# Kernel tuning notes

Hardware: AMD Instinct MI355X
Metric: run time of the kernel (lower is better)

The kernel has to match this reference:

```python
import jax, jax.numpy as jnp
import numpy as np

E = 16          # embed_dim
EPS = 1e-5      # BatchNorm eps


def _lin(x, w, b):
    # torch nn.Linear: y = x @ W^T + b
    return x @ w.T + b


def _mha_len1(v, in_w, in_b, out_w, out_b):
    # nn.MultiheadAttention with query/key/value of seq_len 1:
    # softmax over a single key is identically 1, so the output is
    # out_proj(v_proj(value)) and is independent of query/key.
    wv, bv = in_w[2 * E:3 * E], in_b[2 * E:3 * E]
    return _lin(_lin(v, wv, bv), out_w, out_b)


def _forward(x, ehr_w, ehr_b, img_w, img_b, bio_w, bio_b,
             bio_qkv_w, bio_qkv_b, ehr_qkv_w, ehr_qkv_b, img_qkv_w, img_qkv_b,
             attn_in_w, attn_in_b, attn_out_w, attn_out_b,
             ab_proj_w, ab_proj_b, f1_w, f1_b, bn_g, bn_b, f2_w, f2_b):
    # per-modality scalar -> embed_dim encoders (seq_len-1, so work in [B,E])
    ehr_feat = jax.nn.relu(_lin(x[:, 0:1], ehr_w, ehr_b))  # [B,E]
    img_feat = jax.nn.relu(_lin(x[:, 1:2], img_w, img_b))
    bio_feat = jax.nn.relu(_lin(x[:, 2:3], bio_w, bio_b))

    # stacked q/k/v projections per modality; only V slices affect the output
    bio_qkv = _lin(bio_feat, bio_qkv_w, bio_qkv_b)  # [B,3E]
    ehr_qkv = _lin(ehr_feat, ehr_qkv_w, ehr_qkv_b)
    img_qkv = _lin(img_feat, img_qkv_w, img_qkv_b)
    Va = bio_qkv[:, 2 * E:3 * E]
    Vb = ehr_qkv[:, 2 * E:3 * E]

    bio_ehr = _mha_len1(Vb, attn_in_w, attn_in_b, attn_out_w, attn_out_b)
    ehr_bio = _mha_len1(Va, attn_in_w, attn_in_b, attn_out_w, attn_out_b)

    ab = _lin(jnp.concatenate([bio_ehr, ehr_bio], axis=-1), ab_proj_w, ab_proj_b)  # [B,E]
    img_ab = _mha_len1(ab, attn_in_w, attn_in_b, attn_out_w, attn_out_b)

    final = jnp.concatenate([ab, img_ab], axis=-1)  # [B,2E]
    h = _lin(final, f1_w, f1_b)                      # [B,64]
    # BatchNorm1d, training-mode batch statistics (biased variance); dropout off
    mu = jnp.mean(h, axis=0)
    var = jnp.mean(jnp.square(h - mu), axis=0)
    h = (h - mu) * jax.lax.rsqrt(var + EPS) * bn_g + bn_b
    h = jax.nn.relu(h)
    return _lin(h, f2_w, f2_b)  # [B,3]


def setup_inputs() -> dict:
    key = jax.random.key(0)
    ks = iter(jax.random.split(key, 40))
    w = lambda *shape: jax.random.normal(next(ks), shape, jnp.float32) * 0.1
    B = 1048576
    return {
        "x": jax.random.normal(next(ks), (B, 3), jnp.float32),
        "ehr_w": w(E, 1), "ehr_b": w(E),
        "img_w": w(E, 1), "img_b": w(E),
        "bio_w": w(E, 1), "bio_b": w(E),
        "bio_qkv_w": w(3 * E, E), "bio_qkv_b": w(3 * E),
        "ehr_qkv_w": w(3 * E, E), "ehr_qkv_b": w(3 * E),
        "img_qkv_w": w(3 * E, E), "img_qkv_b": w(3 * E),
        "attn_in_w": w(3 * E, E), "attn_in_b": w(3 * E),
        "attn_out_w": w(E, E), "attn_out_b": w(E),
        "ab_proj_w": w(E, 2 * E), "ab_proj_b": w(E),
        "f1_w": w(64, 2 * E), "f1_b": w(64),
        "bn_g": jnp.ones((64,), jnp.float32), "bn_b": jnp.zeros((64,), jnp.float32),
        "f2_w": w(3, 64), "f2_b": w(3),
    }


def reference(x, ehr_w, ehr_b, img_w, img_b, bio_w, bio_b,
              bio_qkv_w, bio_qkv_b, ehr_qkv_w, ehr_qkv_b, img_qkv_w, img_qkv_b,
              attn_in_w, attn_in_b, attn_out_w, attn_out_b,
              ab_proj_w, ab_proj_b, f1_w, f1_b, bn_g, bn_b, f2_w, f2_b):
    return _forward(x, ehr_w, ehr_b, img_w, img_b, bio_w, bio_b,
                    bio_qkv_w, bio_qkv_b, ehr_qkv_w, ehr_qkv_b, img_qkv_w, img_qkv_b,
                    attn_in_w, attn_in_b, attn_out_w, attn_out_b,
                    ab_proj_w, ab_proj_b, f1_w, f1_b, bn_g, bn_b, f2_w, f2_b)
```

## Files before the change

kernel.cpp:

```cpp
#include <hip/hip_runtime.h>
#include <math.h>

#define NITV 17
#define NCELL (NITV*NITV)
#define NREP 4
#define QS   4096.0f
#define QINV (1.0/4096.0)
#define CELLF 6
#define AGG_N (NCELL*CELLF)
#define PSTRIDE 1760
#define NG 16

#define RAW_OFF   0
#define THR_OFF   4352
#define F2PK_OFF  4384
#define EVT_OFF   4480
#define BVT_OFF   5568
#define ST2_OFF   6656
#define PART_OFF  62976

typedef _Float16 h2 __attribute__((ext_vector_type(2)));

#if __has_builtin(__builtin_amdgcn_fdot2)
__device__ __forceinline__ float fdot2f(h2 a, h2 b, float c) {
  return __builtin_amdgcn_fdot2(a, b, c, false);
}
#else
__device__ __forceinline__ float fdot2f(h2 a, h2 b, float c) {
  return fmaf((float)a.x, (float)b.x, fmaf((float)a.y, (float)b.y, c));
}
#endif

__device__ __forceinline__ int bsearch17(const float* t, float x) {
  bool c8 = t[7] < x;
  float s2 = c8 ? t[11] : t[3];
  bool c4 = s2 < x;
  float sa = c8 ? t[13] : t[5];
  float sb = c8 ? t[9]  : t[1];
  float s3 = c4 ? sa : sb;
  bool c2 = s3 < x;
  float v00 = c2 ? t[2]  : t[0];
  float v01 = c2 ? t[6]  : t[4];
  float v10 = c2 ? t[10] : t[8];
  float v11 = c2 ? t[14] : t[12];
  float w0 = c4 ? v01 : v00;
  float w1 = c4 ? v11 : v10;
  float s4 = c8 ? w1 : w0;
  bool c1 = s4 < x;
  int c = (c8?8:0) + (c4?4:0) + (c2?2:0) + (c1?1:0);
  c += (t[15] < x) ? 1 : 0;
  return c;
}

__global__ void __launch_bounds__(256) hist_kernel(
    const float* __restrict__ x,
    const float* __restrict__ ehr_w, const float* __restrict__ ehr_b,
    const float* __restrict__ bio_w, const float* __restrict__ bio_b,
    const float* __restrict__ bio_qkv_w, const float* __restrict__ bio_qkv_b,
    const float* __restrict__ ehr_qkv_w, const float* __restrict__ ehr_qkv_b,
    const float* __restrict__ attn_in_w, const float* __restrict__ attn_in_b,
    const float* __restrict__ attn_out_w, const float* __restrict__ attn_out_b,
    const float* __restrict__ ab_proj_w, const float* __restrict__ ab_proj_b,
    const float* __restrict__ f1_w, const float* __restrict__ f1_b,
    float* __restrict__ ws, int* __restrict__ partials,
    int B, int nbh)
{
  __shared__ int accS[NREP*AGG_N];
  __shared__ float thrS[32];
  __shared__ float mvec[16], uvec[16], vvec[16], cab[16], h0p[64];
  __shared__ float wEx[16], bEx[16], cEx[16], tEx[16];
  __shared__ float wBx[16], bBx[16], cBx[16], tBx[16];
  __shared__ int   rkE[16], rkB[16];
  const int tid = threadIdx.x;

  if ((int)blockIdx.x == nbh) {
    float* S  = (float*)accS;
    float* M  = S;
    float* P1 = S + 256;
    float* P2 = S + 512;
    float* Ae = S + 768;
    float* Ab = S + 1024;
    float* G  = S + 1280;
    float* Ge = S + 2304;
    float* Gb = S + 3328;

    {
      int o = tid >> 4, k = tid & 15;
      float s = 0.f;
      for (int j = 0; j < 16; ++j)
        s = fmaf(attn_out_w[o*16+j], attn_in_w[(32+j)*16+k], s);
      M[tid] = s;
    }
    if (tid < 16) {
      float s = attn_out_b[tid];
      for (int j = 0; j < 16; ++j)
        s = fmaf(attn_out_w[tid*16+j], attn_in_b[32+j], s);
      mvec[tid] = s;
    }
    __syncthreads();

    {
      int o = tid >> 4, i = tid & 15;
      float s1 = 0.f, s2 = 0.f;
      for (int t = 0; t < 16; ++t) {
        float mt = M[t*16+i];
        s1 = fmaf(ab_proj_w[o*32+t],    mt, s1);
        s2 = fmaf(ab_proj_w[o*32+16+t], mt, s2);
      }
      P1[tid] = s1; P2[tid] = s2;
    }
    if (tid < 16) {
      float su = mvec[tid], sv = mvec[tid];
      for (int i = 0; i < 16; ++i) {
        float mt = M[tid*16+i];
        su = fmaf(mt, ehr_qkv_b[32+i], su);
        sv = fmaf(mt, bio_qkv_b[32+i], sv);
      }
      uvec[tid] = su; vvec[tid] = sv;
    }
    for (int idx = tid; idx < 1024; idx += 256) {
      int j = idx >> 4, k = idx & 15;
      float s = f1_w[j*32+k];
      for (int i = 0; i < 16; ++i)
        s = fmaf(f1_w[j*32+16+i], M[i*16+k], s);
      G[idx] = s;
    }
    __syncthreads();

    {
      int o = tid >> 4, k = tid & 15;
      float s1 = 0.f, s2 = 0.f;
      for (int i = 0; i < 16; ++i) {
        s1 = fmaf(P1[o*16+i], ehr_qkv_w[(32+i)*16+k], s1);
        s2 = fmaf(P2[o*16+i], bio_qkv_w[(32+i)*16+k], s2);
      }
      Ae[tid] = s1; Ab[tid] = s2;
    }
    if (tid < 16) {
      float s = ab_proj_b[tid];
      for (int t = 0; t < 16; ++t) {
        s = fmaf(ab_proj_w[tid*32+t],    uvec[t], s);
        s = fmaf(ab_proj_w[tid*32+16+t], vvec[t], s);
      }
      cab[tid] = s;
    }
    if (tid < 16) {
      float w = ehr_w[tid], b = ehr_b[tid];
      bool z = (w == 0.0f);
      wEx[tid] = z ? 0.f : w;
      bEx[tid] = z ? 0.f : b;
      cEx[tid] = z ? fmaxf(b, 0.f) : 0.f;
      tEx[tid] = z ? __builtin_inff() : (-b / w);
    } else if (tid < 32) {
      int k = tid - 16;
      float w = bio_w[k], b = bio_b[k];
      bool z = (w == 0.0f);
      wBx[k] = z ? 0.f : w;
      bBx[k] = z ? 0.f : b;
      cBx[k] = z ? fmaxf(b, 0.f) : 0.f;
      tBx[k] = z ? __builtin_inff() : (-b / w);
    }
    __syncthreads();

    for (int idx = tid; idx < 1024; idx += 256) {
      int j = idx >> 4, k = idx & 15;
      float s1 = 0.f, s2 = 0.f;
      for (int i = 0; i < 16; ++i) {
        float g = G[j*16+i];
        s1 = fmaf(g, Ae[i*16+k], s1);
        s2 = fmaf(g, Ab[i*16+k], s2);
      }
      Ge[idx] = s1; Gb[idx] = s2;
    }
    if (tid < 64) {
      float s = f1_b[tid];
      for (int i = 0; i < 16; ++i) {
        s = fmaf(G[tid*16+i], cab[i], s);
        s = fmaf(f1_w[tid*32+16+i], mvec[i], s);
      }
      h0p[tid] = s;
    }
    if (tid < 16) {
      int r = 0;
      for (int j = 0; j < 16; ++j)
        r += (tEx[j] < tEx[tid]) || (tEx[j] == tEx[tid] && j < tid);
      rkE[tid] = r;
    } else if (tid < 32) {
      int k = tid - 16, r = 0;
      for (int j = 0; j < 16; ++j)
        r += (tBx[j] < tBx[k]) || (tBx[j] == tBx[k] && j < k);
      rkB[k] = r;
    }
    __syncthreads();

    if (tid < 64) {
      float s = h0p[tid];
      for (int k = 0; k < 16; ++k)
        s += Ge[tid*16+k]*cEx[k] + Gb[tid*16+k]*cBx[k];
      h0p[tid] = s;
    }
    __syncthreads();

    for (int idx = tid; idx < NITV*64; idx += 256) {
      int i = idx >> 6, j = idx & 63;
      float ue = 0.f, ve = 0.f, ub = 0.f, vb = 0.f;
      for (int k = 0; k < 16; ++k) {
        bool actE = (wEx[k] > 0.f) ? (rkE[k] < i) : (rkE[k] >= i);
        bool actB = (wBx[k] > 0.f) ? (rkB[k] < i) : (rkB[k] >= i);
        if (actE) { ue = fmaf(Ge[j*16+k], wEx[k], ue); ve = fmaf(Ge[j*16+k], bEx[k], ve); }
        if (actB) { ub = fmaf(Gb[j*16+k], wBx[k], ub); vb = fmaf(Gb[j*16+k], bBx[k], vb); }
      }
      ws[RAW_OFF + idx]        = ue;
      ws[RAW_OFF + 1088 + idx] = ve + h0p[j];
      ws[RAW_OFF + 2176 + idx] = ub;
      ws[RAW_OFF + 3264 + idx] = vb;
    }
    if (tid < 16) {
      ws[THR_OFF + rkE[tid]]      = tEx[tid];
      ws[THR_OFF + 16 + rkB[tid]] = tBx[tid];
    }
    return;
  }

  if (tid < 16) {
    float tloc[16];
    #pragma unroll
    for (int j = 0; j < 16; ++j) {
      float w = ehr_w[j], b = ehr_b[j];
      tloc[j] = (w == 0.0f) ? __builtin_inff() : (-b / w);
    }
    float mine = tloc[tid];
    int r = 0;
    #pragma unroll
    for (int j = 0; j < 16; ++j)
      r += (tloc[j] < mine) || (tloc[j] == mine && j < tid);
    thrS[r] = mine;
  } else if (tid < 32) {
    int k = tid - 16;
    float tloc[16];
    #pragma unroll
    for (int j = 0; j < 16; ++j) {
      float w = bio_w[j], b = bio_b[j];
      tloc[j] = (w == 0.0f) ? __builtin_inff() : (-b / w);
    }
    float mine = tloc[k];
    int r = 0;
    #pragma unroll
    for (int j = 0; j < 16; ++j)
      r += (tloc[j] < mine) || (tloc[j] == mine && j < k);
    thrS[16 + r] = mine;
  }
  for (int i = tid; i < NREP*AGG_N; i += 256) accS[i] = 0;
  __syncthreads();

  float te[16], tb[16];
  #pragma unroll
  for (int k = 0; k < 16; ++k) { te[k] = thrS[k]; tb[k] = thrS[16+k]; }
  const int rep = tid & (NREP-1);
  const int i4max = (B + 3) >> 2;

  for (int i4 = blockIdx.x*256 + tid; i4 < i4max; i4 += nbh*256) {
    const int s0 = i4*4;
    float xs0[4], xs2[4];
    int nv = 0;
    if (s0 + 4 <= B) {
      const float4* xp = (const float4*)(x + (size_t)s0*3);
      float4 a = xp[0], b = xp[1], c = xp[2];
      xs0[0]=a.x; xs2[0]=a.z;  xs0[1]=a.w; xs2[1]=b.y;
      xs0[2]=b.z; xs2[2]=c.x;  xs0[3]=c.y; xs2[3]=c.w;
      nv = 4;
    } else {
      for (int u = 0; u < 4; ++u) {
        int i = s0 + u;
        if (i < B) { xs0[nv] = x[3*(size_t)i]; xs2[nv] = x[3*(size_t)i+2]; ++nv; }
      }
    }
    for (int u = 0; u < nv; ++u) {
      float x0 = xs0[u], x2 = xs2[u];
      int iv0 = bsearch17(te, x0);
      int iv2 = bsearch17(tb, x2);
      int* c = &accS[rep*AGG_N + (iv0*NITV + iv2)*CELLF];
      atomicAdd(c+0, 1);
      atomicAdd(c+1, __float2int_rn(x0*QS));
      atomicAdd(c+2, __float2int_rn(x2*QS));
      atomicAdd(c+3, __float2int_rn(x0*x0*QS));
      atomicAdd(c+4, __float2int_rn(x2*x2*QS));
      atomicAdd(c+5, __float2int_rn(x0*x2*QS));
    }
  }
  __syncthreads();
  int* out = partials + (size_t)blockIdx.x*PSTRIDE;
  for (int i = tid; i < AGG_N; i += 256)
    out[i] = (accS[i] + accS[AGG_N+i]) + (accS[2*AGG_N+i] + accS[3*AGG_N+i]);
}

__global__ void __launch_bounds__(256) reduce_kernel(
    const int* __restrict__ partials, long long* __restrict__ stage2, int nbh)
{
  const int c = blockIdx.x % 7, g = blockIdx.x / 7;
  const int f = c*256 + threadIdx.x;
  if (f >= AGG_N) { if (f < PSTRIDE) stage2[(size_t)g*PSTRIDE + f] = 0; return; }
  long long s = 0;
  for (int b = g; b < nbh; b += NG)
    s += (long long)partials[(size_t)b*PSTRIDE + f];
  stage2[(size_t)g*PSTRIDE + f] = s;
}

__global__ void __launch_bounds__(256) mid_kernel(
    const long long* __restrict__ stage2,
    float* ws, unsigned int* wsu,
    const float* __restrict__ bn_g, const float* __restrict__ bn_b,
    const float* __restrict__ f2_w, int B)
{
  __shared__ double aggd[AGG_N];
  __shared__ float  Rl[4352];
  __shared__ double sh2p[256];
  __shared__ double margnE[NITV], margxE[NITV], margnB[NITV], margxB[NITV];
  __shared__ float  sArr[64], aE[64], aB[64];
  const int tid = threadIdx.x;

  for (int i = tid; i < 1088; i += 256)
    ((uint4*)Rl)[i] = ((const uint4*)(ws + RAW_OFF))[i];
  for (int i = tid; i < AGG_N; i += 256) {
    long long v = 0;
    #pragma unroll
    for (int g = 0; g < NG; ++g) v += stage2[(size_t)g*PSTRIDE + i];
    aggd[i] = (i % CELLF == 0) ? (double)v : (double)v * QINV;
  }
  __syncthreads();

  if (tid < NITV) {
    double n = 0, sx = 0;
    for (int q = 0; q < NITV; ++q) {
      n  += aggd[(tid*NITV+q)*CELLF];
      sx += aggd[(tid*NITV+q)*CELLF + 1];
    }
    margnE[tid] = n; margxE[tid] = sx;
  } else if (tid >= 32 && tid < 32+NITV) {
    int q = tid - 32;
    double n = 0, sx = 0;
    for (int p = 0; p < NITV; ++p) {
      n  += aggd[(p*NITV+q)*CELLF];
      sx += aggd[(p*NITV+q)*CELLF + 2];
    }
    margnB[q] = n; margxB[q] = sx;
  }

  {
    const int j = tid & 63, pg = tid >> 6;
    double sh2 = 0;
    for (int p = pg; p < NITV; p += 4) {
      const double Ue = (double)Rl[p*64+j];
      const double Ve = (double)Rl[1088 + p*64+j];
      for (int q = 0; q < NITV; ++q) {
        const double* c = &aggd[(p*NITV+q)*CELLF];
        double n = c[0], sx0 = c[1], sx2 = c[2], s00 = c[3], s22 = c[4], s02 = c[5];
        double Ub = (double)Rl[2176 + q*64+j];
        double Vb = (double)Rl[3264 + q*64+j];
        sh2 += s00*Ue*Ue + 2.0*sx0*Ue*Ve + n*Ve*Ve
             + s22*Ub*Ub + 2.0*sx2*Ub*Vb + n*Vb*Vb
             + 2.0*(s02*Ue*Ub + sx0*Ue*Vb + sx2*Ve*Ub + n*Ve*Vb);
      }
    }
    sh2p[tid] = sh2;
  }
  __syncthreads();

  if (tid < 64) {
    const int j = tid;
    double sh2 = (sh2p[j] + sh2p[64+j]) + (sh2p[128+j] + sh2p[192+j]);
    const double invB = 1.0 / (double)B;
    double mua = 0, mub = 0;
    for (int p = 0; p < NITV; ++p) {
      mua += margxE[p]*(double)Rl[p*64+j]      + margnE[p]*(double)Rl[1088+p*64+j];
      mub += margxB[p]*(double)Rl[2176+p*64+j] + margnB[p]*(double)Rl[3264+p*64+j];
    }
    mua *= invB; mub *= invB;
    double mu  = mua + mub;
    double var = sh2*invB - mu*mu;
    double s   = (double)bn_g[j] / sqrt(var + 1e-5);
    sArr[j] = (float)s;
    aE[j] = (float)(0.5*(double)bn_b[j] - s*mua);
    aB[j] = (float)(0.5*(double)bn_b[j] - s*mub);
  }
  __syncthreads();

  for (int idx = tid; idx < NITV*32; idx += 256) {
    int itv = idx >> 5, p = idx & 31;
    int j0 = 2*p, j1 = 2*p + 1;
    float sc0 = sArr[j0], sc1 = sArr[j1];
    h2 U, V;
    U.x = (_Float16)(sc0 * Rl[itv*64+j0]);
    U.y = (_Float16)(sc1 * Rl[itv*64+j1]);
    V.x = (_Float16)(fmaf(sc0, Rl[1088+itv*64+j0], aE[j0]));
    V.y = (_Float16)(fmaf(sc1, Rl[1088+itv*64+j1], aE[j1]));
    wsu[EVT_OFF + p*34 + 2*itv]     = __builtin_bit_cast(unsigned int, U);
    wsu[EVT_OFF + p*34 + 2*itv + 1] = __builtin_bit_cast(unsigned int, V);
    U.x = (_Float16)(sc0 * Rl[2176+itv*64+j0]);
    U.y = (_Float16)(sc1 * Rl[2176+itv*64+j1]);
    V.x = (_Float16)(fmaf(sc0, Rl[3264+itv*64+j0], aB[j0]));
    V.y = (_Float16)(fmaf(sc1, Rl[3264+itv*64+j1], aB[j1]));
    wsu[BVT_OFF + p*34 + 2*itv]     = __builtin_bit_cast(unsigned int, U);
    wsu[BVT_OFF + p*34 + 2*itv + 1] = __builtin_bit_cast(unsigned int, V);
  }
  if (tid < 96) {
    int c = tid >> 5, p = tid & 31;
    h2 F;
    F.x = (_Float16)f2_w[c*64 + 2*p];
    F.y = (_Float16)f2_w[c*64 + 2*p + 1];
    wsu[F2PK_OFF + tid] = __builtin_bit_cast(unsigned int, F);
  }
}

__global__ void __launch_bounds__(256) apply_kernel(
    const float* __restrict__ x, const float* __restrict__ ws,
    const unsigned int* __restrict__ wsu,
    const float* __restrict__ f2_b,
    float* __restrict__ out, int B)
{
  __shared__ __align__(16) unsigned int tabs[2176];
  const int tid = threadIdx.x;

  const int s0 = (blockIdx.x*256 + tid)*4;
  float xs0[4], xs2[4];
  int nv = 0;
  if (s0 + 4 <= B) {
    const float4* xp = (const float4*)(x + (size_t)s0*3);
    float4 a = xp[0], b = xp[1], c = xp[2];
    xs0[0]=a.x; xs2[0]=a.z;  xs0[1]=a.w; xs2[1]=b.y;
    xs0[2]=b.z; xs2[2]=c.x;  xs0[3]=c.y; xs2[3]=c.w;
    nv = 4;
  } else {
    for (int u = 0; u < 4; ++u) {
      int i = s0 + u;
      if (i < B) { xs0[nv] = x[3*(size_t)i]; xs2[nv] = x[3*(size_t)i+2]; ++nv; }
    }
  }

  for (int i = tid; i < 544; i += 256)
    ((uint4*)tabs)[i] = ((const uint4*)(wsu + EVT_OFF))[i];

  float te[16], tb[16];
  #pragma unroll
  for (int k = 0; k < 16; ++k) { te[k] = ws[THR_OFF+k]; tb[k] = ws[THR_OFF+16+k]; }
  const h2* f2h = (const h2*)(wsu + F2PK_OFF);
  const float b0 = f2_b[0], b1 = f2_b[1], b2 = f2_b[2];
  __syncthreads();

  h2 hz; hz.x = (_Float16)0.f; hz.y = (_Float16)0.f;
  float res[12];
  #pragma unroll
  for (int u = 0; u < 4; ++u) {
    if (u >= nv) break;
    float x0 = xs0[u], x2 = xs2[u];
    int iv0 = bsearch17(te, x0);
    int iv2 = bsearch17(tb, x2);
    const uint2* ev = ((const uint2*)tabs) + iv0;
    const uint2* bv = ((const uint2*)(tabs + 1088)) + iv2;
    h2 x0h; x0h.x = (_Float16)x0; x0h.y = (_Float16)x0;
    h2 x2h; x2h.x = (_Float16)x2; x2h.y = (_Float16)x2;
    float a0 = b0, a1 = b1, a2 = b2;
    #pragma unroll
    for (int p = 0; p < 32; ++p) {
      uint2 e = ev[p*NITV];
      uint2 v = bv[p*NITV];
      h2 hA = __builtin_elementwise_fma(x0h, __builtin_bit_cast(h2, e.x),
                                              __builtin_bit_cast(h2, e.y));
      h2 hB = __builtin_elementwise_fma(x2h, __builtin_bit_cast(h2, v.x),
                                              __builtin_bit_cast(h2, v.y));
      h2 hh = hA + hB;
      h2 r  = __builtin_elementwise_max(hh, hz);
      a0 = fdot2f(r, f2h[p],      a0);
      a1 = fdot2f(r, f2h[32 + p], a1);
      a2 = fdot2f(r, f2h[64 + p], a2);
    }
    res[u*3+0] = a0; res[u*3+1] = a1; res[u*3+2] = a2;
  }
  if (nv == 4) {
    float4* op = (float4*)(out + (size_t)s0*3);
    op[0] = make_float4(res[0], res[1], res[2],  res[3]);
    op[1] = make_float4(res[4], res[5], res[6],  res[7]);
    op[2] = make_float4(res[8], res[9], res[10], res[11]);
  } else {
    for (int u = 0; u < nv; ++u) {
      size_t i = (size_t)(s0 + u);
      out[3*i+0] = res[u*3+0]; out[3*i+1] = res[u*3+1]; out[3*i+2] = res[u*3+2];
    }
  }
}

extern "C" void kernel_launch(void* const* d_in, const int* in_sizes, int n_in,
                              void* d_out, int out_size, void* d_ws, size_t ws_size,
                              hipStream_t stream) {
  const float* x          = (const float*)d_in[0];
  const float* ehr_w      = (const float*)d_in[1];
  const float* ehr_b      = (const float*)d_in[2];
  const float* bio_w      = (const float*)d_in[5];
  const float* bio_b      = (const float*)d_in[6];
  const float* bio_qkv_w  = (const float*)d_in[7];
  const float* bio_qkv_b  = (const float*)d_in[8];
  const float* ehr_qkv_w  = (const float*)d_in[9];
  const float* ehr_qkv_b  = (const float*)d_in[10];
  const float* attn_in_w  = (const float*)d_in[13];
  const float* attn_in_b  = (const float*)d_in[14];
  const float* attn_out_w = (const float*)d_in[15];
  const float* attn_out_b = (const float*)d_in[16];
  const float* ab_proj_w  = (const float*)d_in[17];
  const float* ab_proj_b  = (const float*)d_in[18];
  const float* f1_w       = (const float*)d_in[19];
  const float* f1_b       = (const float*)d_in[20];
  const float* bn_g       = (const float*)d_in[21];
  const float* bn_b       = (const float*)d_in[22];
  const float* f2_w       = (const float*)d_in[23];
  const float* f2_b       = (const float*)d_in[24];
  float* out = (float*)d_out;
  float* ws  = (float*)d_ws;
  unsigned int* wsu = (unsigned int*)d_ws;
  int* partials = (int*)d_ws + PART_OFF;
  long long* stage2 = (long long*)((int*)d_ws + ST2_OFF);
  const int B = in_sizes[0] / 3;

  long long avail = (long long)(ws_size / 4) - PART_OFF;
  int nbh = (int)(avail / PSTRIDE);
  if (nbh > 1024) nbh = 1024;
  if (nbh < 128)  nbh = 128;

  hist_kernel<<<nbh+1, 256, 0, stream>>>(x, ehr_w, ehr_b, bio_w, bio_b,
      bio_qkv_w, bio_qkv_b, ehr_qkv_w, ehr_qkv_b,
      attn_in_w, attn_in_b, attn_out_w, attn_out_b,
      ab_proj_w, ab_proj_b, f1_w, f1_b, ws, partials, B, nbh);
  reduce_kernel<<<7*NG, 256, 0, stream>>>(partials, stage2, nbh);
  mid_kernel<<<1, 256, 0, stream>>>(stage2, ws, wsu, bn_g, bn_b, f2_w, B);
  apply_kernel<<<(B + 1023)/1024, 256, 0, stream>>>(x, ws, wsu, f2_b, out, B);
}
```

Before: 76.76 us.

## Fuse four-kernel pipeline into one cooperative persistent kernel with grid syncs

```diff
diff --git a/kernel.cpp b/kernel.cpp
--- a/kernel.cpp
+++ b/kernel.cpp
@@ -1,5 +1,8 @@
 #include <hip/hip_runtime.h>
+#include <hip/hip_cooperative_groups.h>
 #include <math.h>
+
+namespace cg = cooperative_groups;
 
 #define NITV 17
 #define NCELL (NITV*NITV)
@@ -52,176 +55,178 @@
   return c;
 }
 
-__global__ void __launch_bounds__(256) hist_kernel(
-    const float* __restrict__ x,
-    const float* __restrict__ ehr_w, const float* __restrict__ ehr_b,
-    const float* __restrict__ bio_w, const float* __restrict__ bio_b,
-    const float* __restrict__ bio_qkv_w, const float* __restrict__ bio_qkv_b,
-    const float* __restrict__ ehr_qkv_w, const float* __restrict__ ehr_qkv_b,
-    const float* __restrict__ attn_in_w, const float* __restrict__ attn_in_b,
-    const float* __restrict__ attn_out_w, const float* __restrict__ attn_out_b,
-    const float* __restrict__ ab_proj_w, const float* __restrict__ ab_proj_b,
-    const float* __restrict__ f1_w, const float* __restrict__ f1_b,
-    float* __restrict__ ws, int* __restrict__ partials,
-    int B, int nbh)
-{
-  __shared__ int accS[NREP*AGG_N];
-  __shared__ float thrS[32];
-  __shared__ float mvec[16], uvec[16], vvec[16], cab[16], h0p[64];
-  __shared__ float wEx[16], bEx[16], cEx[16], tEx[16];
-  __shared__ float wBx[16], bBx[16], cBx[16], tBx[16];
-  __shared__ int   rkE[16], rkB[16];
-  const int tid = threadIdx.x;
-
-  if ((int)blockIdx.x == nbh) {
-    float* S  = (float*)accS;
-    float* M  = S;
-    float* P1 = S + 256;
-    float* P2 = S + 512;
-    float* Ae = S + 768;
-    float* Ab = S + 1024;
-    float* G  = S + 1280;
-    float* Ge = S + 2304;
-    float* Gb = S + 3328;
-
-    {
-      int o = tid >> 4, k = tid & 15;
-      float s = 0.f;
-      for (int j = 0; j < 16; ++j)
-        s = fmaf(attn_out_w[o*16+j], attn_in_w[(32+j)*16+k], s);
-      M[tid] = s;
-    }
-    if (tid < 16) {
-      float s = attn_out_b[tid];
-      for (int j = 0; j < 16; ++j)
-        s = fmaf(attn_out_w[tid*16+j], attn_in_b[32+j], s);
-      mvec[tid] = s;
-    }
-    __syncthreads();
-
-    {
-      int o = tid >> 4, i = tid & 15;
-      float s1 = 0.f, s2 = 0.f;
-      for (int t = 0; t < 16; ++t) {
-        float mt = M[t*16+i];
-        s1 = fmaf(ab_proj_w[o*32+t],    mt, s1);
-        s2 = fmaf(ab_proj_w[o*32+16+t], mt, s2);
-      }
-      P1[tid] = s1; P2[tid] = s2;
-    }
-    if (tid < 16) {
-      float su = mvec[tid], sv = mvec[tid];
-      for (int i = 0; i < 16; ++i) {
-        float mt = M[tid*16+i];
-        su = fmaf(mt, ehr_qkv_b[32+i], su);
-        sv = fmaf(mt, bio_qkv_b[32+i], sv);
-      }
-      uvec[tid] = su; vvec[tid] = sv;
-    }
-    for (int idx = tid; idx < 1024; idx += 256) {
-      int j = idx >> 4, k = idx & 15;
-      float s = f1_w[j*32+k];
-      for (int i = 0; i < 16; ++i)
-        s = fmaf(f1_w[j*32+16+i], M[i*16+k], s);
-      G[idx] = s;
-    }
-    __syncthreads();
-
-    {
-      int o = tid >> 4, k = tid & 15;
-      float s1 = 0.f, s2 = 0.f;
-      for (int i = 0; i < 16; ++i) {
-        s1 = fmaf(P1[o*16+i], ehr_qkv_w[(32+i)*16+k], s1);
-        s2 = fmaf(P2[o*16+i], bio_qkv_w[(32+i)*16+k], s2);
-      }
-      Ae[tid] = s1; Ab[tid] = s2;
-    }
-    if (tid < 16) {
-      float s = ab_proj_b[tid];
-      for (int t = 0; t < 16; ++t) {
-        s = fmaf(ab_proj_w[tid*32+t],    uvec[t], s);
-        s = fmaf(ab_proj_w[tid*32+16+t], vvec[t], s);
-      }
-      cab[tid] = s;
-    }
-    if (tid < 16) {
-      float w = ehr_w[tid], b = ehr_b[tid];
-      bool z = (w == 0.0f);
-      wEx[tid] = z ? 0.f : w;
-      bEx[tid] = z ? 0.f : b;
-      cEx[tid] = z ? fmaxf(b, 0.f) : 0.f;
-      tEx[tid] = z ? __builtin_inff() : (-b / w);
-    } else if (tid < 32) {
-      int k = tid - 16;
-      float w = bio_w[k], b = bio_b[k];
-      bool z = (w == 0.0f);
-      wBx[k] = z ? 0.f : w;
-      bBx[k] = z ? 0.f : b;
-      cBx[k] = z ? fmaxf(b, 0.f) : 0.f;
-      tBx[k] = z ? __builtin_inff() : (-b / w);
-    }
-    __syncthreads();
-
-    for (int idx = tid; idx < 1024; idx += 256) {
-      int j = idx >> 4, k = idx & 15;
-      float s1 = 0.f, s2 = 0.f;
-      for (int i = 0; i < 16; ++i) {
-        float g = G[j*16+i];
-        s1 = fmaf(g, Ae[i*16+k], s1);
-        s2 = fmaf(g, Ab[i*16+k], s2);
-      }
-      Ge[idx] = s1; Gb[idx] = s2;
-    }
-    if (tid < 64) {
-      float s = f1_b[tid];
-      for (int i = 0; i < 16; ++i) {
-        s = fmaf(G[tid*16+i], cab[i], s);
-        s = fmaf(f1_w[tid*32+16+i], mvec[i], s);
-      }
-      h0p[tid] = s;
-    }
-    if (tid < 16) {
-      int r = 0;
-      for (int j = 0; j < 16; ++j)
-        r += (tEx[j] < tEx[tid]) || (tEx[j] == tEx[tid] && j < tid);
-      rkE[tid] = r;
-    } else if (tid < 32) {
-      int k = tid - 16, r = 0;
-      for (int j = 0; j < 16; ++j)
-        r += (tBx[j] < tBx[k]) || (tBx[j] == tBx[k] && j < k);
-      rkB[k] = r;
-    }
-    __syncthreads();
-
-    if (tid < 64) {
-      float s = h0p[tid];
-      for (int k = 0; k < 16; ++k)
-        s += Ge[tid*16+k]*cEx[k] + Gb[tid*16+k]*cBx[k];
-      h0p[tid] = s;
-    }
-    __syncthreads();
-
-    for (int idx = tid; idx < NITV*64; idx += 256) {
-      int i = idx >> 6, j = idx & 63;
-      float ue = 0.f, ve = 0.f, ub = 0.f, vb = 0.f;
-      for (int k = 0; k < 16; ++k) {
-        bool actE = (wEx[k] > 0.f) ? (rkE[k] < i) : (rkE[k] >= i);
-        bool actB = (wBx[k] > 0.f) ? (rkB[k] < i) : (rkB[k] >= i);
-        if (actE) { ue = fmaf(Ge[j*16+k], wEx[k], ue); ve = fmaf(Ge[j*16+k], bEx[k], ve); }
-        if (actB) { ub = fmaf(Gb[j*16+k], wBx[k], ub); vb = fmaf(Gb[j*16+k], bBx[k], vb); }
-      }
-      ws[RAW_OFF + idx]        = ue;
-      ws[RAW_OFF + 1088 + idx] = ve + h0p[j];
-      ws[RAW_OFF + 2176 + idx] = ub;
-      ws[RAW_OFF + 3264 + idx] = vb;
-    }
-    if (tid < 16) {
-      ws[THR_OFF + rkE[tid]]      = tEx[tid];
-      ws[THR_OFF + 16 + rkB[tid]] = tBx[tid];
-    }
-    return;
-  }
-
+
+__device__ void do_setup(unsigned char* smem, int tid,
+    const float* ehr_w, const float* ehr_b, const float* bio_w, const float* bio_b,
+    const float* bio_qkv_w, const float* bio_qkv_b,
+    const float* ehr_qkv_w, const float* ehr_qkv_b,
+    const float* attn_in_w, const float* attn_in_b,
+    const float* attn_out_w, const float* attn_out_b,
+    const float* ab_proj_w, const float* ab_proj_b,
+    const float* f1_w, const float* f1_b, float* ws)
+{
+  float* S  = (float*)smem;
+  float* M  = S;
+  float* P1 = S + 256;
+  float* P2 = S + 512;
+  float* Ae = S + 768;
+  float* Ab = S + 1024;
+  float* G  = S + 1280;
+  float* Ge = S + 2304;
+  float* Gb = S + 3328;
+  float* aux  = (float*)(smem + 17408);
+  float* mvec = aux;        float* uvec = aux + 16;  float* vvec = aux + 32;
+  float* cab  = aux + 48;   float* h0p  = aux + 64;
+  float* wEx  = aux + 128;  float* bEx  = aux + 144; float* cEx = aux + 160;
+  float* tEx  = aux + 176;  float* wBx  = aux + 192; float* bBx = aux + 208;
+  float* cBx  = aux + 224;  float* tBx  = aux + 240;
+  int*   rkE  = (int*)(aux + 256);
+  int*   rkB  = (int*)(aux + 272);
+
+  {
+    int o = tid >> 4, k = tid & 15;
+    float s = 0.f;
+    for (int j = 0; j < 16; ++j)
+      s = fmaf(attn_out_w[o*16+j], attn_in_w[(32+j)*16+k], s);
+    M[tid] = s;
+  }
+  if (tid < 16) {
+    float s = attn_out_b[tid];
+    for (int j = 0; j < 16; ++j)
+      s = fmaf(attn_out_w[tid*16+j], attn_in_b[32+j], s);
+    mvec[tid] = s;
+  }
+  __syncthreads();
+
+  {
+    int o = tid >> 4, i = tid & 15;
+    float s1 = 0.f, s2 = 0.f;
+    for (int t = 0; t < 16; ++t) {
+      float mt = M[t*16+i];
+      s1 = fmaf(ab_proj_w[o*32+t],    mt, s1);
+      s2 = fmaf(ab_proj_w[o*32+16+t], mt, s2);
+    }
+    P1[tid] = s1; P2[tid] = s2;
+  }
+  if (tid < 16) {
+    float su = mvec[tid], sv = mvec[tid];
+    for (int i = 0; i < 16; ++i) {
+      float mt = M[tid*16+i];
+      su = fmaf(mt, ehr_qkv_b[32+i], su);
+      sv = fmaf(mt, bio_qkv_b[32+i], sv);
+    }
+    uvec[tid] = su; vvec[tid] = sv;
+  }
+  for (int idx = tid; idx < 1024; idx += 256) {
+    int j = idx >> 4, k = idx & 15;
+    float s = f1_w[j*32+k];
+    for (int i = 0; i < 16; ++i)
+      s = fmaf(f1_w[j*32+16+i], M[i*16+k], s);
+    G[idx] = s;
+  }
+  __syncthreads();
+
+  {
+    int o = tid >> 4, k = tid & 15;
+    float s1 = 0.f, s2 = 0.f;
+    for (int i = 0; i < 16; ++i) {
+      s1 = fmaf(P1[o*16+i], ehr_qkv_w[(32+i)*16+k], s1);
+      s2 = fmaf(P2[o*16+i], bio_qkv_w[(32+i)*16+k], s2);
+    }
+    Ae[tid] = s1; Ab[tid] = s2;
+  }
+  if (tid < 16) {
+    float s = ab_proj_b[tid];
+    for (int t = 0; t < 16; ++t) {
+      s = fmaf(ab_proj_w[tid*32+t],    uvec[t], s);
+      s = fmaf(ab_proj_w[tid*32+16+t], vvec[t], s);
+    }
+    cab[tid] = s;
+  }
+  if (tid < 16) {
+    float w = ehr_w[tid], b = ehr_b[tid];
+    bool z = (w == 0.0f);
+    wEx[tid] = z ? 0.f : w;
+    bEx[tid] = z ? 0.f : b;
+    cEx[tid] = z ? fmaxf(b, 0.f) : 0.f;
+    tEx[tid] = z ? __builtin_inff() : (-b / w);
+  } else if (tid < 32) {
+    int k = tid - 16;
+    float w = bio_w[k], b = bio_b[k];
+    bool z = (w == 0.0f);
+    wBx[k] = z ? 0.f : w;
+    bBx[k] = z ? 0.f : b;
+    cBx[k] = z ? fmaxf(b, 0.f) : 0.f;
+    tBx[k] = z ? __builtin_inff() : (-b / w);
+  }
+  __syncthreads();
+
+  for (int idx = tid; idx < 1024; idx += 256) {
+    int j = idx >> 4, k = idx & 15;
+    float s1 = 0.f, s2 = 0.f;
+    for (int i = 0; i < 16; ++i) {
+      float g = G[j*16+i];
+      s1 = fmaf(g, Ae[i*16+k], s1);
+      s2 = fmaf(g, Ab[i*16+k], s2);
+    }
+    Ge[idx] = s1; Gb[idx] = s2;
+  }
+  if (tid < 64) {
+    float s = f1_b[tid];
+    for (int i = 0; i < 16; ++i) {
+      s = fmaf(G[tid*16+i], cab[i], s);
+      s = fmaf(f1_w[tid*32+16+i], mvec[i], s);
+    }
+    h0p[tid] = s;
+  }
+  if (tid < 16) {
+    int r = 0;
+    for (int j = 0; j < 16; ++j)
+      r += (tEx[j] < tEx[tid]) || (tEx[j] == tEx[tid] && j < tid);
+    rkE[tid] = r;
+  } else if (tid < 32) {
+    int k = tid - 16, r = 0;
+    for (int j = 0; j < 16; ++j)
+      r += (tBx[j] < tBx[k]) || (tBx[j] == tBx[k] && j < k);
+    rkB[k] = r;
+  }
+  __syncthreads();
+
+  if (tid < 64) {
+    float s = h0p[tid];
+    for (int k = 0; k < 16; ++k)
+      s += Ge[tid*16+k]*cEx[k] + Gb[tid*16+k]*cBx[k];
+    h0p[tid] = s;
+  }
+  __syncthreads();
+
+  for (int idx = tid; idx < NITV*64; idx += 256) {
+    int i = idx >> 6, j = idx & 63;
+    float ue = 0.f, ve = 0.f, ub = 0.f, vb = 0.f;
+    for (int k = 0; k < 16; ++k) {
+      bool actE = (wEx[k] > 0.f) ? (rkE[k] < i) : (rkE[k] >= i);
+      bool actB = (wBx[k] > 0.f) ? (rkB[k] < i) : (rkB[k] >= i);
+      if (actE) { ue = fmaf(Ge[j*16+k], wEx[k], ue); ve = fmaf(Ge[j*16+k], bEx[k], ve); }
+      if (actB) { ub = fmaf(Gb[j*16+k], wBx[k], ub); vb = fmaf(Gb[j*16+k], bBx[k], vb); }
+    }
+    ws[RAW_OFF + idx]        = ue;
+    ws[RAW_OFF + 1088 + idx] = ve + h0p[j];
+    ws[RAW_OFF + 2176 + idx] = ub;
+    ws[RAW_OFF + 3264 + idx] = vb;
+  }
+  if (tid < 16) {
+    ws[THR_OFF + rkE[tid]]      = tEx[tid];
+    ws[THR_OFF + 16 + rkB[tid]] = tBx[tid];
+  }
+}
+
+__device__ void do_hist(unsigned char* smem, int tid, int bid, int nbh,
+    const float* x, const float* ehr_w, const float* ehr_b,
+    const float* bio_w, const float* bio_b,
+    int* partials, int B)
+{
+  int* accS = (int*)smem;
+  float* thrS = (float*)(smem + 27744);
   if (tid < 16) {
     float tloc[16];
     #pragma unroll
@@ -250,16 +255,21 @@
       r += (tloc[j] < mine) || (tloc[j] == mine && j < k);
     thrS[16 + r] = mine;
   }
-  for (int i = tid; i < NREP*AGG_N; i += 256) accS[i] = 0;
+  {
+    int4 z4 = make_int4(0,0,0,0);
+    int4* a4 = (int4*)accS;
+    for (int i = tid; i < (NREP*AGG_N)/4; i += 256) a4[i] = z4;
+  }
   __syncthreads();
 
   float te[16], tb[16];
   #pragma unroll
   for (int k = 0; k < 16; ++k) { te[k] = thrS[k]; tb[k] = thrS[16+k]; }
   const int rep = tid & (NREP-1);
+  int* const base = &accS[rep*AGG_N];
   const int i4max = (B + 3) >> 2;
 
-  for (int i4 = blockIdx.x*256 + tid; i4 < i4max; i4 += nbh*256) {
+  for (int i4 = bid*256 + tid; i4 < i4max; i4 += nbh*256) {
     const int s0 = i4*4;
     float xs0[4], xs2[4];
     int nv = 0;
@@ -279,7 +289,7 @@
       float x0 = xs0[u], x2 = xs2[u];
       int iv0 = bsearch17(te, x0);
       int iv2 = bsearch17(tb, x2);
-      int* c = &accS[rep*AGG_N + (iv0*NITV + iv2)*CELLF];
+      int* c = base + (iv0*NITV + iv2)*CELLF;
       atomicAdd(c+0, 1);
       atomicAdd(c+1, __float2int_rn(x0*QS));
       atomicAdd(c+2, __float2int_rn(x2*QS));
@@ -289,35 +299,37 @@
     }
   }
   __syncthreads();
-  int* out = partials + (size_t)blockIdx.x*PSTRIDE;
+  int* po = partials + (size_t)bid*PSTRIDE;
   for (int i = tid; i < AGG_N; i += 256)
-    out[i] = (accS[i] + accS[AGG_N+i]) + (accS[2*AGG_N+i] + accS[3*AGG_N+i]);
-}
-
-__global__ void __launch_bounds__(256) reduce_kernel(
-    const int* __restrict__ partials, long long* __restrict__ stage2, int nbh)
-{
-  const int c = blockIdx.x % 7, g = blockIdx.x / 7;
-  const int f = c*256 + threadIdx.x;
-  if (f >= AGG_N) { if (f < PSTRIDE) stage2[(size_t)g*PSTRIDE + f] = 0; return; }
+    po[i] = (accS[i] + accS[AGG_N+i]) + (accS[2*AGG_N+i] + accS[3*AGG_N+i]);
+}
+
+__device__ void do_reduce(int bid, int tid, const int* partials,
+                          long long* stage2, int nbh)
+{
+  const int c = bid % 7, g = bid / 7;
+  const int f = c*256 + tid;
+  if (f >= AGG_N) return;
   long long s = 0;
   for (int b = g; b < nbh; b += NG)
     s += (long long)partials[(size_t)b*PSTRIDE + f];
   stage2[(size_t)g*PSTRIDE + f] = s;
 }
 
-__global__ void __launch_bounds__(256) mid_kernel(
-    const long long* __restrict__ stage2,
-    float* ws, unsigned int* wsu,
-    const float* __restrict__ bn_g, const float* __restrict__ bn_b,
-    const float* __restrict__ f2_w, int B)
-{
-  __shared__ double aggd[AGG_N];
-  __shared__ float  Rl[4352];
-  __shared__ double sh2p[256];
-  __shared__ double margnE[NITV], margxE[NITV], margnB[NITV], margxB[NITV];
-  __shared__ float  sArr[64], aE[64], aB[64];
-  const int tid = threadIdx.x;
+__device__ void do_mid(unsigned char* smem, int tid,
+    const long long* stage2, float* ws, unsigned int* wsu,
+    const float* bn_g, const float* bn_b, const float* f2_w, int B)
+{
+  float*  aggf = (float*)smem;
+  float*  Rl   = (float*)(smem + 6944);
+  double* sh2p = (double*)(smem + 24352);
+  double* margnE = (double*)(smem + 26400);
+  double* margxE = margnE + NITV;
+  double* margnB = margxE + NITV;
+  double* margxB = margnB + NITV;
+  float*  sArr = (float*)(smem + 26944);
+  float*  aE   = sArr + 64;
+  float*  aB   = sArr + 128;
 
   for (int i = tid; i < 1088; i += 256)
     ((uint4*)Rl)[i] = ((const uint4*)(ws + RAW_OFF))[i];
@@ -325,23 +337,23 @@
     long long v = 0;
     #pragma unroll
     for (int g = 0; g < NG; ++g) v += stage2[(size_t)g*PSTRIDE + i];
-    aggd[i] = (i % CELLF == 0) ? (double)v : (double)v * QINV;
+    aggf[i] = (i % CELLF == 0) ? (float)v : (float)((double)v * QINV);
   }
   __syncthreads();
 
   if (tid < NITV) {
     double n = 0, sx = 0;
     for (int q = 0; q < NITV; ++q) {
-      n  += aggd[(tid*NITV+q)*CELLF];
-      sx += aggd[(tid*NITV+q)*CELLF + 1];
+      n  += (double)aggf[(tid*NITV+q)*CELLF];
+      sx += (double)aggf[(tid*NITV+q)*CELLF + 1];
     }
     margnE[tid] = n; margxE[tid] = sx;
   } else if (tid >= 32 && tid < 32+NITV) {
     int q = tid - 32;
     double n = 0, sx = 0;
     for (int p = 0; p < NITV; ++p) {
-      n  += aggd[(p*NITV+q)*CELLF];
-      sx += aggd[(p*NITV+q)*CELLF + 2];
+      n  += (double)aggf[(p*NITV+q)*CELLF];
+      sx += (double)aggf[(p*NITV+q)*CELLF + 2];
     }
     margnB[q] = n; margxB[q] = sx;
   }
@@ -353,7 +365,7 @@
       const double Ue = (double)Rl[p*64+j];
       const double Ve = (double)Rl[1088 + p*64+j];
       for (int q = 0; q < NITV; ++q) {
-        const double* c = &aggd[(p*NITV+q)*CELLF];
+        const float* c = &aggf[(p*NITV+q)*CELLF];
         double n = c[0], sx0 = c[1], sx2 = c[2], s00 = c[3], s22 = c[4], s02 = c[5];
         double Ub = (double)Rl[2176 + q*64+j];
         double Vb = (double)Rl[3264 + q*64+j];
@@ -412,31 +424,11 @@
   }
 }
 
-__global__ void __launch_bounds__(256) apply_kernel(
-    const float* __restrict__ x, const float* __restrict__ ws,
-    const unsigned int* __restrict__ wsu,
-    const float* __restrict__ f2_b,
-    float* __restrict__ out, int B)
-{
-  __shared__ __align__(16) unsigned int tabs[2176];
-  const int tid = threadIdx.x;
-
-  const int s0 = (blockIdx.x*256 + tid)*4;
-  float xs0[4], xs2[4];
-  int nv = 0;
-  if (s0 + 4 <= B) {
-    const float4* xp = (const float4*)(x + (size_t)s0*3);
-    float4 a = xp[0], b = xp[1], c = xp[2];
-    xs0[0]=a.x; xs2[0]=a.z;  xs0[1]=a.w; xs2[1]=b.y;
-    xs0[2]=b.z; xs2[2]=c.x;  xs0[3]=c.y; xs2[3]=c.w;
-    nv = 4;
-  } else {
-    for (int u = 0; u < 4; ++u) {
-      int i = s0 + u;
-      if (i < B) { xs0[nv] = x[3*(size_t)i]; xs2[nv] = x[3*(size_t)i+2]; ++nv; }
-    }
-  }
-
+__device__ void do_apply(unsigned char* smem, int tid, int bid, int nblk,
+    const float* x, const float* ws, const unsigned int* wsu,
+    const float* f2_b, float* out, int B)
+{
+  unsigned int* tabs = (unsigned int*)smem;
   for (int i = tid; i < 544; i += 256)
     ((uint4*)tabs)[i] = ((const uint4*)(wsu + EVT_OFF))[i];
 
@@ -448,45 +440,153 @@
   __syncthreads();
 
   h2 hz; hz.x = (_Float16)0.f; hz.y = (_Float16)0.f;
-  float res[12];
-  #pragma unroll
-  for (int u = 0; u < 4; ++u) {
-    if (u >= nv) break;
-    float x0 = xs0[u], x2 = xs2[u];
-    int iv0 = bsearch17(te, x0);
-    int iv2 = bsearch17(tb, x2);
-    const uint2* ev = ((const uint2*)tabs) + iv0;
-    const uint2* bv = ((const uint2*)(tabs + 1088)) + iv2;
-    h2 x0h; x0h.x = (_Float16)x0; x0h.y = (_Float16)x0;
-    h2 x2h; x2h.x = (_Float16)x2; x2h.y = (_Float16)x2;
-    float a0 = b0, a1 = b1, a2 = b2;
+  const int i4max = (B + 3) >> 2;
+  for (int i4 = bid*256 + tid; i4 < i4max; i4 += nblk*256) {
+    const int s0 = i4*4;
+    float xs0[4], xs2[4];
+    int nv = 0;
+    if (s0 + 4 <= B) {
+      const float4* xp = (const float4*)(x + (size_t)s0*3);
+      float4 a = xp[0], b = xp[1], c = xp[2];
+      xs0[0]=a.x; xs2[0]=a.z;  xs0[1]=a.w; xs2[1]=b.y;
+      xs0[2]=b.z; xs2[2]=c.x;  xs0[3]=c.y; xs2[3]=c.w;
+      nv = 4;
+    } else {
+      for (int u = 0; u < 4; ++u) {
+        int i = s0 + u;
+        if (i < B) { xs0[nv] = x[3*(size_t)i]; xs2[nv] = x[3*(size_t)i+2]; ++nv; }
+      }
+    }
+    float res[12];
     #pragma unroll
-    for (int p = 0; p < 32; ++p) {
-      uint2 e = ev[p*NITV];
-      uint2 v = bv[p*NITV];
-      h2 hA = __builtin_elementwise_fma(x0h, __builtin_bit_cast(h2, e.x),
-                                              __builtin_bit_cast(h2, e.y));
-      h2 hB = __builtin_elementwise_fma(x2h, __builtin_bit_cast(h2, v.x),
-                                              __builtin_bit_cast(h2, v.y));
-      h2 hh = hA + hB;
-      h2 r  = __builtin_elementwise_max(hh, hz);
-      a0 = fdot2f(r, f2h[p],      a0);
-      a1 = fdot2f(r, f2h[32 + p], a1);
-      a2 = fdot2f(r, f2h[64 + p], a2);
-    }
-    res[u*3+0] = a0; res[u*3+1] = a1; res[u*3+2] = a2;
-  }
-  if (nv == 4) {
-    float4* op = (float4*)(out + (size_t)s0*3);
-    op[0] = make_float4(res[0], res[1], res[2],  res[3]);
-    op[1] = make_float4(res[4], res[5], res[6],  res[7]);
-    op[2] = make_float4(res[8], res[9], res[10], res[11]);
-  } else {
-    for (int u = 0; u < nv; ++u) {
-      size_t i = (size_t)(s0 + u);
-      out[3*i+0] = res[u*3+0]; out[3*i+1] = res[u*3+1]; out[3*i+2] = res[u*3+2];
-    }
-  }
+    for (int u = 0; u < 4; ++u) {
+      if (u >= nv) break;
+      float x0 = xs0[u], x2 = xs2[u];
+      int iv0 = bsearch17(te, x0);
+      int iv2 = bsearch17(tb, x2);
+      const uint2* ev = ((const uint2*)tabs) + iv0;
+      const uint2* bv = ((const uint2*)(tabs + 1088)) + iv2;
+      h2 x0h; x0h.x = (_Float16)x0; x0h.y = (_Float16)x0;
+      h2 x2h; x2h.x = (_Float16)x2; x2h.y = (_Float16)x2;
+      float a0 = b0, a1 = b1, a2 = b2;
+      #pragma unroll
+      for (int p = 0; p < 32; ++p) {
+        uint2 e = ev[p*NITV];
+        uint2 v = bv[p*NITV];
+        h2 hA = __builtin_elementwise_fma(x0h, __builtin_bit_cast(h2, e.x),
+                                                __builtin_bit_cast(h2, e.y));
+        h2 hB = __builtin_elementwise_fma(x2h, __builtin_bit_cast(h2, v.x),
+                                                __builtin_bit_cast(h2, v.y));
+        h2 hh = hA + hB;
+        h2 r  = __builtin_elementwise_max(hh, hz);
+        a0 = fdot2f(r, f2h[p],      a0);
+        a1 = fdot2f(r, f2h[32 + p], a1);
+        a2 = fdot2f(r, f2h[64 + p], a2);
+      }
+      res[u*3+0] = a0; res[u*3+1] = a1; res[u*3+2] = a2;
+    }
+    if (nv == 4) {
+      float4* op = (float4*)(out + (size_t)s0*3);
+      op[0] = make_float4(res[0], res[1], res[2],  res[3]);
+      op[1] = make_float4(res[4], res[5], res[6],  res[7]);
+      op[2] = make_float4(res[8], res[9], res[10], res[11]);
+    } else {
+      for (int u = 0; u < nv; ++u) {
+        size_t i = (size_t)(s0 + u);
+        out[3*i+0] = res[u*3+0]; out[3*i+1] = res[u*3+1]; out[3*i+2] = res[u*3+2];
+      }
+    }
+  }
+}
+
+__global__ void __launch_bounds__(256, 4) fused_all(
+    const float* __restrict__ x,
+    const float* __restrict__ ehr_w, const float* __restrict__ ehr_b,
+    const float* __restrict__ bio_w, const float* __restrict__ bio_b,
+    const float* __restrict__ bio_qkv_w, const float* __restrict__ bio_qkv_b,
+    const float* __restrict__ ehr_qkv_w, const float* __restrict__ ehr_qkv_b,
+    const float* __restrict__ attn_in_w, const float* __restrict__ attn_in_b,
+    const float* __restrict__ attn_out_w, const float* __restrict__ attn_out_b,
+    const float* __restrict__ ab_proj_w, const float* __restrict__ ab_proj_b,
+    const float* __restrict__ f1_w, const float* __restrict__ f1_b,
+    const float* __restrict__ bn_g, const float* __restrict__ bn_b,
+    const float* __restrict__ f2_w, const float* __restrict__ f2_b,
+    float* __restrict__ ws, float* __restrict__ out, int B, int G)
+{
+  __shared__ __align__(16) unsigned char smem[27904];
+  cg::grid_group grid = cg::this_grid();
+  const int tid = threadIdx.x;
+  const int bid = (int)blockIdx.x;
+  unsigned int* wsu = (unsigned int*)ws;
+  int* partials = (int*)ws + PART_OFF;
+  long long* stage2 = (long long*)((int*)ws + ST2_OFF);
+  const int nbh = G - 1;
+
+  if (bid == nbh)
+    do_setup(smem, tid, ehr_w, ehr_b, bio_w, bio_b, bio_qkv_w, bio_qkv_b,
+             ehr_qkv_w, ehr_qkv_b, attn_in_w, attn_in_b, attn_out_w, attn_out_b,
+             ab_proj_w, ab_proj_b, f1_w, f1_b, ws);
+  else
+    do_hist(smem, tid, bid, nbh, x, ehr_w, ehr_b, bio_w, bio_b, partials, B);
+
+  grid.sync();
+
+  if (bid < 7*NG) do_reduce(bid, tid, partials, stage2, nbh);
+
+  grid.sync();
+
+  if (bid == 0) do_mid(smem, tid, stage2, ws, wsu, bn_g, bn_b, f2_w, B);
+
+  grid.sync();
+
+  do_apply(smem, tid, bid, G, x, ws, wsu, f2_b, out, B);
+}
+
+__global__ void __launch_bounds__(256) hist_kernel(
+    const float* __restrict__ x,
+    const float* __restrict__ ehr_w, const float* __restrict__ ehr_b,
+    const float* __restrict__ bio_w, const float* __restrict__ bio_b,
+    const float* __restrict__ bio_qkv_w, const float* __restrict__ bio_qkv_b,
+    const float* __restrict__ ehr_qkv_w, const float* __restrict__ ehr_qkv_b,
+    const float* __restrict__ attn_in_w, const float* __restrict__ attn_in_b,
+    const float* __restrict__ attn_out_w, const float* __restrict__ attn_out_b,
+    const float* __restrict__ ab_proj_w, const float* __restrict__ ab_proj_b,
+    const float* __restrict__ f1_w, const float* __restrict__ f1_b,
+    float* __restrict__ ws, int* __restrict__ partials, int B, int nbh)
+{
+  __shared__ __align__(16) unsigned char smem[27904];
+  const int tid = threadIdx.x;
+  if ((int)blockIdx.x == nbh)
+    do_setup(smem, tid, ehr_w, ehr_b, bio_w, bio_b, bio_qkv_w, bio_qkv_b,
+             ehr_qkv_w, ehr_qkv_b, attn_in_w, attn_in_b, attn_out_w, attn_out_b,
+             ab_proj_w, ab_proj_b, f1_w, f1_b, ws);
+  else
+    do_hist(smem, tid, (int)blockIdx.x, nbh, x, ehr_w, ehr_b, bio_w, bio_b,
+            partials, B);
+}
+
+__global__ void __launch_bounds__(256) reduce_kernel(
+    const int* __restrict__ partials, long long* __restrict__ stage2, int nbh)
+{
+  do_reduce((int)blockIdx.x, threadIdx.x, partials, stage2, nbh);
+}
+
+__global__ void __launch_bounds__(256) mid_kernel(
+    const long long* __restrict__ stage2, float* ws, unsigned int* wsu,
+    const float* __restrict__ bn_g, const float* __restrict__ bn_b,
+    const float* __restrict__ f2_w, int B)
+{
+  __shared__ __align__(16) unsigned char smem[27744];
+  do_mid(smem, threadIdx.x, stage2, ws, wsu, bn_g, bn_b, f2_w, B);
+}
+
+__global__ void __launch_bounds__(256) apply_kernel(
+    const float* __restrict__ x, const float* __restrict__ ws,
+    const unsigned int* __restrict__ wsu, const float* __restrict__ f2_b,
+    float* __restrict__ out, int B, int nblk)
+{
+  __shared__ __align__(16) unsigned char smem[8704];
+  do_apply(smem, threadIdx.x, (int)blockIdx.x, nblk, x, ws, wsu, f2_b, out, B);
 }
 
 extern "C" void kernel_launch(void* const* d_in, const int* in_sizes, int n_in,
@@ -518,18 +618,44 @@
   unsigned int* wsu = (unsigned int*)d_ws;
   int* partials = (int*)d_ws + PART_OFF;
   long long* stage2 = (long long*)((int*)d_ws + ST2_OFF);
-  const int B = in_sizes[0] / 3;
+  int B = in_sizes[0] / 3;
 
   long long avail = (long long)(ws_size / 4) - PART_OFF;
-  int nbh = (int)(avail / PSTRIDE);
-  if (nbh > 1024) nbh = 1024;
-  if (nbh < 128)  nbh = 128;
-
-  hist_kernel<<<nbh+1, 256, 0, stream>>>(x, ehr_w, ehr_b, bio_w, bio_b,
-      bio_qkv_w, bio_qkv_b, ehr_qkv_w, ehr_qkv_b,
-      attn_in_w, attn_in_b, attn_out_w, attn_out_b,
-      ab_proj_w, ab_proj_b, f1_w, f1_b, ws, partials, B, nbh);
-  reduce_kernel<<<7*NG, 256, 0, stream>>>(partials, stage2, nbh);
-  mid_kernel<<<1, 256, 0, stream>>>(stage2, ws, wsu, bn_g, bn_b, f2_w, B);
-  apply_kernel<<<(B + 1023)/1024, 256, 0, stream>>>(x, ws, wsu, f2_b, out, B);
-}
+  int cap = (int)(avail / PSTRIDE);
+  if (cap > 1023) cap = 1023;
+
+  int nbPerCU = 0;
+  hipError_t qe = hipOccupancyMaxActiveBlocksPerMultiprocessor(
+      &nbPerCU, (const void*)fused_all, 256, 0);
+  int G = (qe == hipSuccess) ? nbPerCU * 256 : 0;
+  if (G > 1024) G = 1024;
+  if (G - 1 > cap) G = cap + 1;
+
+  hipError_t e = hipErrorUnknown;
+  if (G >= 160) {
+    void* args[] = {
+      (void*)&x,
+      (void*)&ehr_w, (void*)&ehr_b, (void*)&bio_w, (void*)&bio_b,
+      (void*)&bio_qkv_w, (void*)&bio_qkv_b, (void*)&ehr_qkv_w, (void*)&ehr_qkv_b,
+      (void*)&attn_in_w, (void*)&attn_in_b, (void*)&attn_out_w, (void*)&attn_out_b,
+      (void*)&ab_proj_w, (void*)&ab_proj_b, (void*)&f1_w, (void*)&f1_b,
+      (void*)&bn_g, (void*)&bn_b, (void*)&f2_w, (void*)&f2_b,
+      (void*)&ws, (void*)&out, (void*)&B, (void*)&G
+    };
+    e = hipLaunchCooperativeKernel((const void*)fused_all, dim3(G), dim3(256),
+                                   args, 0, stream);
+  }
+  if (e != hipSuccess) {
+    int nbh = cap;
+    if (nbh > 1023) nbh = 1023;
+    if (nbh < 128)  nbh = 128;
+    hist_kernel<<<nbh+1, 256, 0, stream>>>(x, ehr_w, ehr_b, bio_w, bio_b,
+        bio_qkv_w, bio_qkv_b, ehr_qkv_w, ehr_qkv_b,
+        attn_in_w, attn_in_b, attn_out_w, attn_out_b,
+        ab_proj_w, ab_proj_b, f1_w, f1_b, ws, partials, B, nbh);
+    reduce_kernel<<<7*NG, 256, 0, stream>>>(partials, stage2, nbh);
+    mid_kernel<<<1, 256, 0, stream>>>(stage2, ws, wsu, bn_g, bn_b, f2_w, B);
+    int nblk = (B + 1023) / 1024;
+    apply_kernel<<<nblk, 256, 0, stream>>>(x, ws, wsu, f2_b, out, B, nblk);
+  }
+}
```

Result: slower. 155.2 us (+102.2%).
